# Performance work log

Hardware: AMD Instinct MI355X
Metric: run time of the kernel (lower is better)

## Reference

```python
import jax, jax.numpy as jnp
import numpy as np

K = 3.0  # power parameter k from __init__

def _weight1_sq(d2, r):
    # weight1 on squared distances: (1 - (d/r)^2)^k where d < r, else 0
    r2 = r * r
    flag = d2 < r2
    base = jnp.where(flag, 1.0 - d2 / r2, 0.0)  # >= 0 where flag
    return jnp.where(flag, base ** K, 0.0)

def _weight2(d, r):
    half = r * 0.5
    in1 = d < half
    in2 = (d >= half) & (d < r)
    d_safe = jnp.where(in2, d, half)  # keep base in [0,1] outside the branch
    t = (2.0 * d_safe - r) / r
    w2 = (1.0 - t * t) ** K
    return jnp.where(in1, 1.0, jnp.where(in2, w2, 0.0))

def _normalize(w):
    return w / jnp.sum(w, axis=0, keepdims=True)


def setup_inputs() -> dict:
    key = jax.random.key(0)
    n, p = 4096, 64
    x = jax.random.normal(key, (n, p), dtype=jnp.float32)
    return {
        "x": x,
        "r0": jnp.float32(12.0),
        "r1": jnp.float32(11.0),
        "r2": jnp.float32(12.0),
    }


def reference(x, r0, r1, r2):
    y = x  # y = x.clone(); purely functional here
    sq = jnp.sum(x * x, axis=1)
    # squared pairwise distances (cdist^2), clamped for numerical safety
    d2 = jnp.maximum(sq[:, None] + sq[None, :] - 2.0 * (x @ x.T), 0.0)  # (n, n)
    max_dist = jnp.sqrt(jnp.max(d2))
    # parameter reassignment r := min(r, max_dist)
    r0 = jnp.minimum(r0, max_dist)
    r1 = jnp.minimum(r1, max_dist)
    r2 = jnp.minimum(r2, max_dist)
    # row selection inds: dist[i,i] = 0 <= r0 always, so all rows are kept (identity)
    alpha = _normalize(_weight1_sq(d2, r0))  # (n, n)
    mu = alpha.T @ x  # (n, p)
    mu = jnp.where(jnp.isnan(mu), y, mu)
    U = y - mu  # (n, p), contraction directions
    # projection[i,j] = c_ij * U_j with c_ij = (x_i - y_j) . U_j
    c = x @ U.T - jnp.sum(y * U, axis=1)[None, :]  # (n, n)
    du = c * c * jnp.sum(U * U, axis=1)[None, :]   # ||projection||^2, (n, n)
    du = jnp.maximum(du, 1e-6)
    dv = jnp.sqrt(jnp.maximum(d2 - du, 1e-6))
    du = jnp.sqrt(du)
    beta = _normalize(_weight2(dv, r1) * _weight2(du, r2))  # (n, n)
    e_Z = beta.T @ x  # (n, p)
    return jnp.where(jnp.isnan(e_Z), y, e_Z)
```

## Files before the change

### kernel.cpp

```cpp
#include <hip/hip_runtime.h>
#include <stdint.h>

typedef unsigned short u16;
typedef short bf16x8 __attribute__((ext_vector_type(8)));
typedef unsigned short u16x4 __attribute__((ext_vector_type(4)));
typedef float f32x4 __attribute__((ext_vector_type(4)));

#define NROW 4096
#define LDW 72
#define SLICE 262144
#define NSPLIT 8

__device__ __forceinline__ u16 f2bf(float f) {
  uint32_t u = __float_as_uint(f);
  u = (u + 0x7fffu + ((u >> 16) & 1u)) >> 16;
  return (u16)u;
}

__device__ __forceinline__ u16 f2bf_t(float f) {
  return (u16)(__float_as_uint(f) >> 16);
}

__device__ __forceinline__ f32x4 mfma16(bf16x8 a, bf16x8 b, f32x4 c) {
  return __builtin_amdgcn_mfma_f32_16x16x32_bf16(a, b, c, 0, 0, 0);
}

__device__ __forceinline__ bf16x8 ld8(const u16* p) {
  return *reinterpret_cast<const bf16x8*>(p);
}

__device__ __forceinline__ float fast_sqrt(float x) {
  return __builtin_amdgcn_sqrtf(x);
}

__device__ __forceinline__ float slots_max(const float* __restrict__ maxslots, int lane) {
  float md = maxslots[lane * 16];
#pragma unroll
  for (int o = 1; o < 64; o <<= 1) md = fmaxf(md, __shfl_xor(md, o));
  return md;
}

__global__ __launch_bounds__(256) void prep_kernel(const float* __restrict__ x,
                                                   u16* __restrict__ xb, u16* __restrict__ xT,
                                                   float* __restrict__ sq,
                                                   float* __restrict__ maxslots) {
  __shared__ u16 lt[64 * 68];
  __shared__ float pmax[4];
  const int w = threadIdx.x >> 6, lane = threadIdx.x & 63;
  const int r0 = blockIdx.x * 64;
  const float x0l = x[lane];
  float wmax = 0.f;
#pragma unroll
  for (int rr = 0; rr < 16; ++rr) {
    int rl = w * 16 + rr;
    int row = r0 + rl;
    float v = x[row * 64 + lane];
    u16 b = f2bf(v);
    xb[row * 64 + lane] = b;
    lt[lane * 68 + rl] = b;
    float s = v * v;
    float d = v - x0l;
    float s2 = d * d;
#pragma unroll
    for (int o = 1; o < 64; o <<= 1) {
      s += __shfl_xor(s, o);
      s2 += __shfl_xor(s2, o);
    }
    if (lane == 0) sq[row] = s;
    wmax = fmaxf(wmax, s2);
  }
  if (lane == 0) pmax[w] = wmax;
  __syncthreads();
#pragma unroll
  for (int cc = 0; cc < 16; ++cc) {
    int c = w * 16 + cc;
    xT[c * NROW + r0 + lane] = lt[c * 68 + lane];
  }
  if (threadIdx.x == 0)
    maxslots[blockIdx.x * 16] = fmaxf(fmaxf(pmax[0], pmax[1]), fmaxf(pmax[2], pmax[3]));
}

__global__ __launch_bounds__(256) void pass1_max(const u16* __restrict__ xb,
                                                 const float* __restrict__ sq,
                                                 float* __restrict__ maxslots,
                                                 const float* __restrict__ r0in,
                                                 const float* __restrict__ r1in,
                                                 const float* __restrict__ r2in) {
  __shared__ float red[4];
  int w = threadIdx.x >> 6, lane = threadIdx.x & 63;
  {
    float lb = slots_max(maxslots, lane);
    float rmax = fmaxf(fmaxf(r0in[0], r1in[0]), r2in[0]);
    if (lb >= rmax * rmax) return;
  }
  int l16 = lane & 15, quad = lane >> 4;
  int ti = blockIdx.x;
  int i0 = ti * 64 + w * 16;
  bf16x8 a0 = ld8(xb + (i0 + l16) * 64 + quad * 8);
  bf16x8 a1 = ld8(xb + (i0 + l16) * 64 + 32 + quad * 8);
  float sqi[4];
#pragma unroll
  for (int r = 0; r < 4; ++r) sqi[r] = sq[i0 + quad * 4 + r];
  float m = 0.f;
  const int jbase = blockIdx.y * 256;
#pragma unroll
  for (int jb = 0; jb < 4; ++jb) {
    int j0 = jbase + jb * 64;
#pragma unroll
    for (int jt = 0; jt < 4; ++jt) {
      int jr = j0 + jt * 16 + l16;
      bf16x8 b0 = ld8(xb + jr * 64 + quad * 8);
      bf16x8 b1 = ld8(xb + jr * 64 + 32 + quad * 8);
      f32x4 g = {0.f, 0.f, 0.f, 0.f};
      g = mfma16(a0, b0, g);
      g = mfma16(a1, b1, g);
      float sj = sq[jr];
#pragma unroll
      for (int r = 0; r < 4; ++r) m = fmaxf(m, fmaf(-2.f, g[r], sqi[r] + sj));
    }
  }
  m = fmaxf(m, 0.f);
#pragma unroll
  for (int o = 1; o < 64; o <<= 1) m = fmaxf(m, __shfl_xor(m, o));
  if (lane == 0) red[w] = m;
  __syncthreads();
  if (threadIdx.x == 0) {
    m = fmaxf(fmaxf(red[0], red[1]), fmaxf(red[2], red[3]));
    atomicMax((int*)&maxslots[ti * 16], __float_as_int(m));
  }
}

__global__ __launch_bounds__(256, 2) void pass2_kernel(
    const u16* __restrict__ xb, const u16* __restrict__ xT, const float* __restrict__ sq,
    const float* __restrict__ maxslots, const float* __restrict__ r0in,
    float* __restrict__ mu_part, float* __restrict__ s_part) {
  __shared__ u16 ldsw[2][64 * LDW];
  __shared__ u16 xjt[64 * LDW];
  __shared__ float sred[4][64];
  const int tid = threadIdx.x, w = tid >> 6, lane = tid & 63;
  const int l16 = lane & 15, quad = lane >> 4;
  const int j0 = blockIdx.x * 64;
  const int ibase = blockIdx.y * 512;

#pragma unroll
  for (int k = 0; k < 2; ++k) {
    int ch = tid + k * 256;
    int row = ch >> 3, c8 = ch & 7;
    *reinterpret_cast<bf16x8*>(&xjt[row * LDW + c8 * 8]) = ld8(xb + (j0 + row) * 64 + c8 * 8);
  }

  const float md = slots_max(maxslots, lane);
  const float r0c = fminf(r0in[0], fast_sqrt(md));
  const float invr0sq = 1.f / (r0c * r0c);

  float sqj[4];
#pragma unroll
  for (int jt = 0; jt < 4; ++jt) sqj[jt] = sq[j0 + jt * 16 + l16];

  f32x4 zero4 = {0.f, 0.f, 0.f, 0.f};
  f32x4 acc[4];
#pragma unroll
  for (int pt = 0; pt < 4; ++pt) acc[pt] = zero4;
  float sa[4] = {0.f, 0.f, 0.f, 0.f};

  auto do_weights = [&](bf16x8 A0, bf16x8 A1, float4 QI, u16* wbuf) {
#pragma unroll
    for (int jp = 0; jp < 2; ++jp) {
      const int jt0 = jp * 2, jt1 = jp * 2 + 1;
      f32x4 g0 = zero4, g1 = zero4;
      bf16x8 x00 = ld8(&xjt[(jt0 * 16 + l16) * LDW + quad * 8]);
      bf16x8 x10 = ld8(&xjt[(jt1 * 16 + l16) * LDW + quad * 8]);
      bf16x8 x01 = ld8(&xjt[(jt0 * 16 + l16) * LDW + 32 + quad * 8]);
      bf16x8 x11 = ld8(&xjt[(jt1 * 16 + l16) * LDW + 32 + quad * 8]);
      g0 = mfma16(A0, x00, g0);
      g1 = mfma16(A0, x10, g1);
      g0 = mfma16(A1, x01, g0);
      g1 = mfma16(A1, x11, g1);
      u16x4 pk0, pk1;
#pragma unroll
      for (int r = 0; r < 4; ++r) {
        float d2a = fmaxf(fmaf(-2.f, g0[r], QI[r] + sqj[jt0]), 0.f);
        float ba = fmaxf(fmaf(-d2a, invr0sq, 1.f), 0.f);
        float wa = ba * ba * ba;
        sa[jt0] += wa;
        pk0[r] = f2bf_t(wa);
        float d2b = fmaxf(fmaf(-2.f, g1[r], QI[r] + sqj[jt1]), 0.f);
        float bb = fmaxf(fmaf(-d2b, invr0sq, 1.f), 0.f);
        float wb = bb * bb * bb;
        sa[jt1] += wb;
        pk1[r] = f2bf_t(wb);
      }
      *reinterpret_cast<u16x4*>(&wbuf[(jt0 * 16 + l16) * LDW + w * 16 + quad * 4]) = pk0;
      *reinterpret_cast<u16x4*>(&wbuf[(jt1 * 16 + l16) * LDW + w * 16 + quad * 4]) = pk1;
    }
  };

  const int ir0 = ibase + w * 16;
  bf16x8 p0 = ld8(xb + (ir0 + l16) * 64 + quad * 8);
  bf16x8 p1 = ld8(xb + (ir0 + l16) * 64 + 32 + quad * 8);
  float4 q0 = *reinterpret_cast<const float4*>(&sq[ir0 + quad * 4]);
  __syncthreads();
  do_weights(p0, p1, q0, &ldsw[0][0]);
  bf16x8 a0 = ld8(xb + (ir0 + 64 + l16) * 64 + quad * 8);
  bf16x8 a1 = ld8(xb + (ir0 + 64 + l16) * 64 + 32 + quad * 8);
  float4 qi = *reinterpret_cast<const float4*>(&sq[ir0 + 64 + quad * 4]);
  __syncthreads();

#pragma unroll
  for (int s = 0; s < 8; ++s) {
    u16* rbuf = &ldsw[s & 1][0];
    const int ib = ibase + s * 64;
    bf16x8 aw0 = ld8(&rbuf[(w * 16 + l16) * LDW + quad * 8]);
    bf16x8 aw1 = ld8(&rbuf[(w * 16 + l16) * LDW + 32 + quad * 8]);
    const u16* xp0 = xT + (0 * 16 + l16) * NROW + ib + quad * 8;
    const u16* xp1 = xT + (1 * 16 + l16) * NROW + ib + quad * 8;
    const u16* xp2 = xT + (2 * 16 + l16) * NROW + ib + quad * 8;
    const u16* xp3 = xT + (3 * 16 + l16) * NROW + ib + quad * 8;
    bf16x8 t00 = ld8(xp0), t01 = ld8(xp0 + 32);
    bf16x8 t10 = ld8(xp1), t11 = ld8(xp1 + 32);
    bf16x8 t20 = ld8(xp2), t21 = ld8(xp2 + 32);
    bf16x8 t30 = ld8(xp3), t31 = ld8(xp3 + 32);
    if (s < 7) {
      do_weights(a0, a1, qi, &ldsw[(s + 1) & 1][0]);
      if (s < 6) {
        const int irn = ibase + (s + 2) * 64 + w * 16;
        a0 = ld8(xb + (irn + l16) * 64 + quad * 8);
        a1 = ld8(xb + (irn + l16) * 64 + 32 + quad * 8);
        qi = *reinterpret_cast<const float4*>(&sq[irn + quad * 4]);
      }
    }
    acc[0] = mfma16(aw0, t00, acc[0]);
    acc[0] = mfma16(aw1, t01, acc[0]);
    acc[1] = mfma16(aw0, t10, acc[1]);
    acc[1] = mfma16(aw1, t11, acc[1]);
    acc[2] = mfma16(aw0, t20, acc[2]);
    acc[2] = mfma16(aw1, t21, acc[2]);
    acc[3] = mfma16(aw0, t30, acc[3]);
    acc[3] = mfma16(aw1, t31, acc[3]);
    __syncthreads();
  }
  float* mp = mu_part + (size_t)blockIdx.y * SLICE;
#pragma unroll
  for (int pt = 0; pt < 4; ++pt)
#pragma unroll
    for (int r = 0; r < 4; ++r)
      mp[(j0 + w * 16 + quad * 4 + r) * 64 + pt * 16 + l16] = acc[pt][r];
#pragma unroll
  for (int jt = 0; jt < 4; ++jt) {
    float v = sa[jt];
    v += __shfl_xor(v, 16);
    v += __shfl_xor(v, 32);
    if (lane < 16) sred[w][jt * 16 + lane] = v;
  }
  __syncthreads();
  if (tid < 64)
    s_part[blockIdx.y * NROW + j0 + tid] =
        sred[0][tid] + sred[1][tid] + sred[2][tid] + sred[3][tid];
}

__global__ __launch_bounds__(256) void finish_mu_kernel(
    const float* __restrict__ x, const float* __restrict__ mu_part,
    const float* __restrict__ s_part, u16* __restrict__ ub, float* __restrict__ un2,
    float* __restrict__ tvec) {
  const int tid = threadIdx.x;
  const int row = blockIdx.x * 16 + (tid >> 4);
  const int c4 = tid & 15;
  float4 num = {0.f, 0.f, 0.f, 0.f};
  float den = 0.f;
#pragma unroll
  for (int y = 0; y < NSPLIT; ++y) {
    float4 v = *reinterpret_cast<const float4*>(&mu_part[(size_t)y * SLICE + row * 64 + c4 * 4]);
    num.x += v.x; num.y += v.y; num.z += v.z; num.w += v.w;
    den += s_part[y * NROW + row];
  }
  float4 xv = *reinterpret_cast<const float4*>(&x[row * 64 + c4 * 4]);
  float inv = 1.f / den;
  float m0 = num.x * inv, m1 = num.y * inv, m2 = num.z * inv, m3 = num.w * inv;
  if (m0 != m0) m0 = xv.x;
  if (m1 != m1) m1 = xv.y;
  if (m2 != m2) m2 = xv.z;
  if (m3 != m3) m3 = xv.w;
  float U0 = xv.x - m0, U1 = xv.y - m1, U2 = xv.z - m2, U3 = xv.w - m3;
  u16x4 pb;
  pb[0] = f2bf(U0); pb[1] = f2bf(U1); pb[2] = f2bf(U2); pb[3] = f2bf(U3);
  *reinterpret_cast<u16x4*>(&ub[row * 64 + c4 * 4]) = pb;
  float a = U0 * U0 + U1 * U1 + U2 * U2 + U3 * U3;
  float b = xv.x * U0 + xv.y * U1 + xv.z * U2 + xv.w * U3;
#pragma unroll
  for (int o = 1; o < 16; o <<= 1) {
    a += __shfl_xor(a, o);
    b += __shfl_xor(b, o);
  }
  if (c4 == 0) {
    un2[row] = a;
    tvec[row] = b;
  }
}

__global__ __launch_bounds__(256, 2) void pass3_kernel(
    const u16* __restrict__ xb, const u16* __restrict__ xT, const u16* __restrict__ ub,
    const float* __restrict__ sq, const float* __restrict__ tvec, const float* __restrict__ un2,
    const float* __restrict__ maxslots, const float* __restrict__ r1in,
    const float* __restrict__ r2in, float* __restrict__ ez_part, float* __restrict__ s_part) {
  __shared__ u16 ldsw[2][64 * LDW];
  __shared__ u16 xjt[64 * LDW];
  __shared__ u16 ujt[64 * LDW];
  __shared__ float sred[4][64];
  const int tid = threadIdx.x, w = tid >> 6, lane = tid & 63;
  const int l16 = lane & 15, quad = lane >> 4;
  const int j0 = blockIdx.x * 64;
  const int ibase = blockIdx.y * 512;

#pragma unroll
  for (int k = 0; k < 2; ++k) {
    int ch = tid + k * 256;
    int row = ch >> 3, c8 = ch & 7;
    *reinterpret_cast<bf16x8*>(&xjt[row * LDW + c8 * 8]) = ld8(xb + (j0 + row) * 64 + c8 * 8);
    *reinterpret_cast<bf16x8*>(&ujt[row * LDW + c8 * 8]) = ld8(ub + (j0 + row) * 64 + c8 * 8);
  }

  const float md = slots_max(maxslots, lane);
  const float mdist = fast_sqrt(md);
  const float r1c = fminf(r1in[0], mdist);
  const float r2c = fminf(r2in[0], mdist);
  const float i1x2 = 2.f / r1c;
  const float i2x2 = 2.f / r2c;

  float sqj[4], tj[4], u2j[4];
#pragma unroll
  for (int jt = 0; jt < 4; ++jt) {
    int jr = j0 + jt * 16 + l16;
    sqj[jt] = sq[jr];
    tj[jt] = tvec[jr];
    u2j[jt] = un2[jr];
  }
  f32x4 zero4 = {0.f, 0.f, 0.f, 0.f};
  f32x4 acc[4];
#pragma unroll
  for (int pt = 0; pt < 4; ++pt) acc[pt] = zero4;
  float sb[4] = {0.f, 0.f, 0.f, 0.f};

  auto do_weights = [&](bf16x8 A0, bf16x8 A1, float4 QI, u16* wbuf) {
#pragma unroll
    for (int jt = 0; jt < 4; ++jt) {
      f32x4 gxx = zero4, gxu = zero4;
      bf16x8 xf0 = ld8(&xjt[(jt * 16 + l16) * LDW + quad * 8]);
      bf16x8 uf0 = ld8(&ujt[(jt * 16 + l16) * LDW + quad * 8]);
      bf16x8 xf1 = ld8(&xjt[(jt * 16 + l16) * LDW + 32 + quad * 8]);
      bf16x8 uf1 = ld8(&ujt[(jt * 16 + l16) * LDW + 32 + quad * 8]);
      gxx = mfma16(A0, xf0, gxx);
      gxu = mfma16(A0, uf0, gxu);
      gxx = mfma16(A1, xf1, gxx);
      gxu = mfma16(A1, uf1, gxu);
      const float tjv = tj[jt], u2jv = u2j[jt], sjv = sqj[jt];
      u16x4 pk;
#pragma unroll
      for (int r = 0; r < 4; ++r) {
        float d2 = fmaxf(fmaf(-2.f, gxx[r], QI[r] + sjv), 0.f);
        float c = gxu[r] - tjv;
        float du2 = fmaxf(c * c * u2jv, 1e-6f);
        float dv2 = fmaxf(d2 - du2, 1e-6f);
        float du = fast_sqrt(du2);
        float dv = fast_sqrt(dv2);
        float q1 = fminf(fmaxf(fmaf(dv, i1x2, -1.f), 0.f), 1.f);
        float b1 = fmaf(-q1, q1, 1.f);
        float w1 = b1 * b1 * b1;
        float q2 = fminf(fmaxf(fmaf(du, i2x2, -1.f), 0.f), 1.f);
        float b2 = fmaf(-q2, q2, 1.f);
        float w2 = b2 * b2 * b2;
        float wv = w1 * w2;
        sb[jt] += wv;
        pk[r] = f2bf_t(wv);
      }
      *reinterpret_cast<u16x4*>(&wbuf[(jt * 16 + l16) * LDW + w * 16 + quad * 4]) = pk;
    }
  };

  const int ir0 = ibase + w * 16;
  bf16x8 p0 = ld8(xb + (ir0 + l16) * 64 + quad * 8);
  bf16x8 p1 = ld8(xb + (ir0 + l16) * 64 + 32 + quad * 8);
  float4 q0 = *reinterpret_cast<const float4*>(&sq[ir0 + quad * 4]);
  __syncthreads();
  do_weights(p0, p1, q0, &ldsw[0][0]);
  bf16x8 a0 = ld8(xb + (ir0 + 64 + l16) * 64 + quad * 8);
  bf16x8 a1 = ld8(xb + (ir0 + 64 + l16) * 64 + 32 + quad * 8);
  float4 qi = *reinterpret_cast<const float4*>(&sq[ir0 + 64 + quad * 4]);
  __syncthreads();

#pragma unroll
  for (int s = 0; s < 8; ++s) {
    u16* rbuf = &ldsw[s & 1][0];
    const int ib = ibase + s * 64;
    bf16x8 aw0 = ld8(&rbuf[(w * 16 + l16) * LDW + quad * 8]);
    bf16x8 aw1 = ld8(&rbuf[(w * 16 + l16) * LDW + 32 + quad * 8]);
    const u16* xp0 = xT + (0 * 16 + l16) * NROW + ib + quad * 8;
    const u16* xp1 = xT + (1 * 16 + l16) * NROW + ib + quad * 8;
    const u16* xp2 = xT + (2 * 16 + l16) * NROW + ib + quad * 8;
    const u16* xp3 = xT + (3 * 16 + l16) * NROW + ib + quad * 8;
    bf16x8 t00 = ld8(xp0), t01 = ld8(xp0 + 32);
    bf16x8 t10 = ld8(xp1), t11 = ld8(xp1 + 32);
    bf16x8 t20 = ld8(xp2), t21 = ld8(xp2 + 32);
    bf16x8 t30 = ld8(xp3), t31 = ld8(xp3 + 32);
    if (s < 7) {
      do_weights(a0, a1, qi, &ldsw[(s + 1) & 1][0]);
      if (s < 6) {
        const int irn = ibase + (s + 2) * 64 + w * 16;
        a0 = ld8(xb + (irn + l16) * 64 + quad * 8);
        a1 = ld8(xb + (irn + l16) * 64 + 32 + quad * 8);
        qi = *reinterpret_cast<const float4*>(&sq[irn + quad * 4]);
      }
    }
    acc[0] = mfma16(aw0, t00, acc[0]);
    acc[0] = mfma16(aw1, t01, acc[0]);
    acc[1] = mfma16(aw0, t10, acc[1]);
    acc[1] = mfma16(aw1, t11, acc[1]);
    acc[2] = mfma16(aw0, t20, acc[2]);
    acc[2] = mfma16(aw1, t21, acc[2]);
    acc[3] = mfma16(aw0, t30, acc[3]);
    acc[3] = mfma16(aw1, t31, acc[3]);
    __syncthreads();
  }
  float* ep = ez_part + (size_t)blockIdx.y * SLICE;
#pragma unroll
  for (int pt = 0; pt < 4; ++pt)
#pragma unroll
    for (int r = 0; r < 4; ++r)
      ep[(j0 + w * 16 + quad * 4 + r) * 64 + pt * 16 + l16] = acc[pt][r];
#pragma unroll
  for (int jt = 0; jt < 4; ++jt) {
    float v = sb[jt];
    v += __shfl_xor(v, 16);
    v += __shfl_xor(v, 32);
    if (lane < 16) sred[w][jt * 16 + lane] = v;
  }
  __syncthreads();
  if (tid < 64)
    s_part[blockIdx.y * NROW + j0 + tid] =
        sred[0][tid] + sred[1][tid] + sred[2][tid] + sred[3][tid];
}

__global__ __launch_bounds__(256) void finish_kernel(const float* __restrict__ x,
                                                     const float* __restrict__ ez_part,
                                                     const float* __restrict__ s_part,
                                                     float* __restrict__ out) {
  const int tid = threadIdx.x;
  const int row = blockIdx.x * 16 + (tid >> 4);
  const int c4 = tid & 15;
  float4 num = {0.f, 0.f, 0.f, 0.f};
  float den = 0.f;
#pragma unroll
  for (int y = 0; y < NSPLIT; ++y) {
    float4 v = *reinterpret_cast<const float4*>(&ez_part[(size_t)y * SLICE + row * 64 + c4 * 4]);
    num.x += v.x; num.y += v.y; num.z += v.z; num.w += v.w;
    den += s_part[y * NROW + row];
  }
  float4 xv = *reinterpret_cast<const float4*>(&x[row * 64 + c4 * 4]);
  float inv = 1.f / den;
  float4 o;
  o.x = num.x * inv; o.y = num.y * inv; o.z = num.z * inv; o.w = num.w * inv;
  if (o.x != o.x) o.x = xv.x;
  if (o.y != o.y) o.y = xv.y;
  if (o.z != o.z) o.z = xv.z;
  if (o.w != o.w) o.w = xv.w;
  *reinterpret_cast<float4*>(&out[row * 64 + c4 * 4]) = o;
}

extern "C" void kernel_launch(void* const* d_in, const int* in_sizes, int n_in,
                              void* d_out, int out_size, void* d_ws, size_t ws_size,
                              hipStream_t stream) {
  (void)in_sizes; (void)n_in; (void)out_size;
  const float* x = (const float*)d_in[0];
  const float* r0 = (const float*)d_in[1];
  const float* r1 = (const float*)d_in[2];
  const float* r2 = (const float*)d_in[3];
  float* out = (float*)d_out;
  char* ws = (char*)d_ws;

  u16* xb = (u16*)(ws);
  u16* xT = (u16*)(ws + (512 << 10));
  u16* ub = (u16*)(ws + (1024 << 10));
  float* sq = (float*)(ws + (1536 << 10));
  float* tv = (float*)(ws + (1552 << 10));
  float* u2 = (float*)(ws + (1568 << 10));
  float* maxslots = (float*)(ws + (1584 << 10));
  float* s_part_a = (float*)(ws + (1588 << 10));
  float* s_part_b = (float*)(ws + (1844 << 10));
  float* part = (float*)(ws + (2100 << 10));
  size_t need = ((size_t)2100 << 10) + ((size_t)8 << 20);
  if (ws_size < need) return;

  prep_kernel<<<64, 256, 0, stream>>>(x, xb, xT, sq, maxslots);
  pass1_max<<<dim3(64, 16), 256, 0, stream>>>(xb, sq, maxslots, r0, r1, r2);
  pass2_kernel<<<dim3(64, NSPLIT), 256, 0, stream>>>(xb, xT, sq, maxslots, r0, part, s_part_a);
  finish_mu_kernel<<<256, 256, 0, stream>>>(x, part, s_part_a, ub, u2, tv);
  pass3_kernel<<<dim3(64, NSPLIT), 256, 0, stream>>>(xb, xT, ub, sq, tv, u2, maxslots, r1, r2,
                                                     part, s_part_b);
  finish_kernel<<<256, 256, 0, stream>>>(x, part, s_part_b, out);
}
```

Measured before the change: 127.3 us.

## Fuse all six passes into one cooperative persistent kernel with grid syncs

Replaces the six separate kernel launches (prep, max pass, mu pass, finish_mu, beta pass, finish) with a single cooperative kernel of 512 blocks that separates the phases with grid.sync(). This removes per-launch overhead and the gaps between kernels. The old multi-kernel path is kept as a fallback if the cooperative launch fails. The cost is six grid-wide barriers, idle blocks in the phases that use fewer blocks, and a dependence on all 512 blocks being co-resident at two blocks per CU.

```diff
diff --git a/kernel.cpp b/kernel.cpp
--- a/kernel.cpp
+++ b/kernel.cpp
@@ -1,5 +1,8 @@
 #include <hip/hip_runtime.h>
+#include <hip/hip_cooperative_groups.h>
 #include <stdint.h>
+
+namespace cg = cooperative_groups;
 
 typedef unsigned short u16;
 typedef short bf16x8 __attribute__((ext_vector_type(8)));
@@ -33,12 +36,421 @@
   return __builtin_amdgcn_sqrtf(x);
 }
 
-__device__ __forceinline__ float slots_max(const float* __restrict__ maxslots, int lane) {
+__device__ __forceinline__ float slots_max(const float* maxslots, int lane) {
   float md = maxslots[lane * 16];
 #pragma unroll
   for (int o = 1; o < 64; o <<= 1) md = fmaxf(md, __shfl_xor(md, o));
   return md;
 }
+
+__global__ __launch_bounds__(256, 2) void fused_all(
+    const float* __restrict__ x, const float* __restrict__ r0in,
+    const float* __restrict__ r1in, const float* __restrict__ r2in,
+    float* __restrict__ out, u16* __restrict__ xb, u16* __restrict__ xT,
+    u16* __restrict__ ub, float* __restrict__ sq, float* __restrict__ tvec,
+    float* __restrict__ un2, float* maxslots, float* __restrict__ s_part_a,
+    float* __restrict__ s_part_b, float* part ) {
+  cg::grid_group grid = cg::this_grid();
+  __shared__ u16 smem[4 * 64 * LDW];
+  __shared__ float sred[4][64];
+  u16* ldsw0 = smem;
+  u16* ldsw1 = smem + 64 * LDW;
+  u16* xjt = smem + 2 * 64 * LDW;
+  u16* ujt = smem + 3 * 64 * LDW;
+  const int gid = blockIdx.x;
+  const int tid = threadIdx.x, w = tid >> 6, lane = tid & 63;
+  const int l16 = lane & 15, quad = lane >> 4;
+  const int j0 = (gid & 63) * 64;
+  const int yb = gid >> 6;
+  const int ibase = yb * 512;
+  f32x4 zero4 = {0.f, 0.f, 0.f, 0.f};
+
+  if (gid < 64) {
+    u16* lt = smem;
+    const int r0 = gid * 64;
+    const float x0l = x[lane];
+    float wmax = 0.f;
+#pragma unroll
+    for (int rr = 0; rr < 16; ++rr) {
+      int rl = w * 16 + rr;
+      int row = r0 + rl;
+      float v = x[row * 64 + lane];
+      u16 b = f2bf(v);
+      xb[row * 64 + lane] = b;
+      lt[lane * 68 + rl] = b;
+      float s = v * v;
+      float d = v - x0l;
+      float s2 = d * d;
+#pragma unroll
+      for (int o = 1; o < 64; o <<= 1) {
+        s += __shfl_xor(s, o);
+        s2 += __shfl_xor(s2, o);
+      }
+      if (lane == 0) sq[row] = s;
+      wmax = fmaxf(wmax, s2);
+    }
+    if (lane == 0) sred[0][w] = wmax;
+    __syncthreads();
+#pragma unroll
+    for (int cc = 0; cc < 16; ++cc) {
+      int c = w * 16 + cc;
+      xT[c * NROW + r0 + lane] = lt[c * 68 + lane];
+    }
+    if (tid == 0)
+      maxslots[gid * 16] =
+          fmaxf(fmaxf(sred[0][0], sred[0][1]), fmaxf(sred[0][2], sred[0][3]));
+  }
+  grid.sync();
+
+  {
+    float lb = slots_max(maxslots, lane);
+    float rmax = fmaxf(fmaxf(r0in[0], r1in[0]), r2in[0]);
+    if (lb < rmax * rmax) {
+      for (int uu = 0; uu < 2; ++uu) {
+        int u = gid * 2 + uu;
+        int ti = u & 63, yy = u >> 6;
+        int i0 = ti * 64 + w * 16;
+        bf16x8 a0 = ld8(xb + (i0 + l16) * 64 + quad * 8);
+        bf16x8 a1 = ld8(xb + (i0 + l16) * 64 + 32 + quad * 8);
+        float sqi[4];
+#pragma unroll
+        for (int r = 0; r < 4; ++r) sqi[r] = sq[i0 + quad * 4 + r];
+        float m = 0.f;
+        const int jbase = yy * 256;
+#pragma unroll
+        for (int jb = 0; jb < 4; ++jb) {
+          int jj0 = jbase + jb * 64;
+#pragma unroll
+          for (int jt = 0; jt < 4; ++jt) {
+            int jr = jj0 + jt * 16 + l16;
+            bf16x8 b0 = ld8(xb + jr * 64 + quad * 8);
+            bf16x8 b1 = ld8(xb + jr * 64 + 32 + quad * 8);
+            f32x4 g = zero4;
+            g = mfma16(a0, b0, g);
+            g = mfma16(a1, b1, g);
+            float sj = sq[jr];
+#pragma unroll
+            for (int r = 0; r < 4; ++r) m = fmaxf(m, fmaf(-2.f, g[r], sqi[r] + sj));
+          }
+        }
+        m = fmaxf(m, 0.f);
+#pragma unroll
+        for (int o = 1; o < 64; o <<= 1) m = fmaxf(m, __shfl_xor(m, o));
+        if (lane == 0) sred[0][w] = m;
+        __syncthreads();
+        if (tid == 0) {
+          m = fmaxf(fmaxf(sred[0][0], sred[0][1]), fmaxf(sred[0][2], sred[0][3]));
+          atomicMax((int*)&maxslots[ti * 16], __float_as_int(m));
+        }
+        __syncthreads();
+      }
+    }
+  }
+  grid.sync();
+
+  {
+#pragma unroll
+    for (int k = 0; k < 2; ++k) {
+      int ch = tid + k * 256;
+      int row = ch >> 3, c8 = ch & 7;
+      *reinterpret_cast<bf16x8*>(&xjt[row * LDW + c8 * 8]) =
+          ld8(xb + (j0 + row) * 64 + c8 * 8);
+    }
+    const float md = slots_max(maxslots, lane);
+    const float r0c = fminf(r0in[0], fast_sqrt(md));
+    const float invr0sq = 1.f / (r0c * r0c);
+    float sqj[4];
+#pragma unroll
+    for (int jt = 0; jt < 4; ++jt) sqj[jt] = sq[j0 + jt * 16 + l16];
+    f32x4 acc[4];
+#pragma unroll
+    for (int pt = 0; pt < 4; ++pt) acc[pt] = zero4;
+    float sa[4] = {0.f, 0.f, 0.f, 0.f};
+    u16* bufs[2] = {ldsw0, ldsw1};
+
+    auto do_weights = [&](bf16x8 A0, bf16x8 A1, float4 QI, u16* wbuf) {
+#pragma unroll
+      for (int jp = 0; jp < 2; ++jp) {
+        const int jt0 = jp * 2, jt1 = jp * 2 + 1;
+        f32x4 g0 = zero4, g1 = zero4;
+        bf16x8 x00 = ld8(&xjt[(jt0 * 16 + l16) * LDW + quad * 8]);
+        bf16x8 x10 = ld8(&xjt[(jt1 * 16 + l16) * LDW + quad * 8]);
+        bf16x8 x01 = ld8(&xjt[(jt0 * 16 + l16) * LDW + 32 + quad * 8]);
+        bf16x8 x11 = ld8(&xjt[(jt1 * 16 + l16) * LDW + 32 + quad * 8]);
+        g0 = mfma16(A0, x00, g0);
+        g1 = mfma16(A0, x10, g1);
+        g0 = mfma16(A1, x01, g0);
+        g1 = mfma16(A1, x11, g1);
+        u16x4 pk0, pk1;
+#pragma unroll
+        for (int r = 0; r < 4; ++r) {
+          float d2a = fmaxf(fmaf(-2.f, g0[r], QI[r] + sqj[jt0]), 0.f);
+          float ba = fmaxf(fmaf(-d2a, invr0sq, 1.f), 0.f);
+          float wa = ba * ba * ba;
+          sa[jt0] += wa;
+          pk0[r] = f2bf_t(wa);
+          float d2b = fmaxf(fmaf(-2.f, g1[r], QI[r] + sqj[jt1]), 0.f);
+          float bb = fmaxf(fmaf(-d2b, invr0sq, 1.f), 0.f);
+          float wb = bb * bb * bb;
+          sa[jt1] += wb;
+          pk1[r] = f2bf_t(wb);
+        }
+        *reinterpret_cast<u16x4*>(&wbuf[(jt0 * 16 + l16) * LDW + w * 16 + quad * 4]) = pk0;
+        *reinterpret_cast<u16x4*>(&wbuf[(jt1 * 16 + l16) * LDW + w * 16 + quad * 4]) = pk1;
+      }
+    };
+
+    const int ir0 = ibase + w * 16;
+    bf16x8 p0 = ld8(xb + (ir0 + l16) * 64 + quad * 8);
+    bf16x8 p1 = ld8(xb + (ir0 + l16) * 64 + 32 + quad * 8);
+    float4 q0 = *reinterpret_cast<const float4*>(&sq[ir0 + quad * 4]);
+    __syncthreads();
+    do_weights(p0, p1, q0, bufs[0]);
+    bf16x8 a0 = ld8(xb + (ir0 + 64 + l16) * 64 + quad * 8);
+    bf16x8 a1 = ld8(xb + (ir0 + 64 + l16) * 64 + 32 + quad * 8);
+    float4 qi = *reinterpret_cast<const float4*>(&sq[ir0 + 64 + quad * 4]);
+    __syncthreads();
+
+#pragma unroll
+    for (int s = 0; s < 8; ++s) {
+      u16* rbuf = bufs[s & 1];
+      const int ib = ibase + s * 64;
+      bf16x8 aw0 = ld8(&rbuf[(w * 16 + l16) * LDW + quad * 8]);
+      bf16x8 aw1 = ld8(&rbuf[(w * 16 + l16) * LDW + 32 + quad * 8]);
+      const u16* xp0 = xT + (0 * 16 + l16) * NROW + ib + quad * 8;
+      const u16* xp1 = xT + (1 * 16 + l16) * NROW + ib + quad * 8;
+      const u16* xp2 = xT + (2 * 16 + l16) * NROW + ib + quad * 8;
+      const u16* xp3 = xT + (3 * 16 + l16) * NROW + ib + quad * 8;
+      bf16x8 t00 = ld8(xp0), t01 = ld8(xp0 + 32);
+      bf16x8 t10 = ld8(xp1), t11 = ld8(xp1 + 32);
+      bf16x8 t20 = ld8(xp2), t21 = ld8(xp2 + 32);
+      bf16x8 t30 = ld8(xp3), t31 = ld8(xp3 + 32);
+      if (s < 7) {
+        do_weights(a0, a1, qi, bufs[(s + 1) & 1]);
+        if (s < 6) {
+          const int irn = ibase + (s + 2) * 64 + w * 16;
+          a0 = ld8(xb + (irn + l16) * 64 + quad * 8);
+          a1 = ld8(xb + (irn + l16) * 64 + 32 + quad * 8);
+          qi = *reinterpret_cast<const float4*>(&sq[irn + quad * 4]);
+        }
+      }
+      acc[0] = mfma16(aw0, t00, acc[0]);
+      acc[0] = mfma16(aw1, t01, acc[0]);
+      acc[1] = mfma16(aw0, t10, acc[1]);
+      acc[1] = mfma16(aw1, t11, acc[1]);
+      acc[2] = mfma16(aw0, t20, acc[2]);
+      acc[2] = mfma16(aw1, t21, acc[2]);
+      acc[3] = mfma16(aw0, t30, acc[3]);
+      acc[3] = mfma16(aw1, t31, acc[3]);
+      __syncthreads();
+    }
+    float* mp = part + (size_t)yb * SLICE;
+#pragma unroll
+    for (int pt = 0; pt < 4; ++pt)
+#pragma unroll
+      for (int r = 0; r < 4; ++r)
+        mp[(j0 + w * 16 + quad * 4 + r) * 64 + pt * 16 + l16] = acc[pt][r];
+#pragma unroll
+    for (int jt = 0; jt < 4; ++jt) {
+      float v = sa[jt];
+      v += __shfl_xor(v, 16);
+      v += __shfl_xor(v, 32);
+      if (lane < 16) sred[w][jt * 16 + lane] = v;
+    }
+    __syncthreads();
+    if (tid < 64)
+      s_part_a[yb * NROW + j0 + tid] =
+          sred[0][tid] + sred[1][tid] + sred[2][tid] + sred[3][tid];
+  }
+  grid.sync();
+
+  if (gid < 256) {
+    const int row = gid * 16 + (tid >> 4);
+    const int c4 = tid & 15;
+    float4 num = {0.f, 0.f, 0.f, 0.f};
+    float den = 0.f;
+#pragma unroll
+    for (int y = 0; y < NSPLIT; ++y) {
+      float4 v = *reinterpret_cast<const float4*>(&part[(size_t)y * SLICE + row * 64 + c4 * 4]);
+      num.x += v.x; num.y += v.y; num.z += v.z; num.w += v.w;
+      den += s_part_a[y * NROW + row];
+    }
+    float4 xv = *reinterpret_cast<const float4*>(&x[row * 64 + c4 * 4]);
+    float inv = 1.f / den;
+    float m0 = num.x * inv, m1 = num.y * inv, m2 = num.z * inv, m3 = num.w * inv;
+    if (m0 != m0) m0 = xv.x;
+    if (m1 != m1) m1 = xv.y;
+    if (m2 != m2) m2 = xv.z;
+    if (m3 != m3) m3 = xv.w;
+    float U0 = xv.x - m0, U1 = xv.y - m1, U2 = xv.z - m2, U3 = xv.w - m3;
+    u16x4 pb;
+    pb[0] = f2bf(U0); pb[1] = f2bf(U1); pb[2] = f2bf(U2); pb[3] = f2bf(U3);
+    *reinterpret_cast<u16x4*>(&ub[row * 64 + c4 * 4]) = pb;
+    float a = U0 * U0 + U1 * U1 + U2 * U2 + U3 * U3;
+    float b = xv.x * U0 + xv.y * U1 + xv.z * U2 + xv.w * U3;
+#pragma unroll
+    for (int o = 1; o < 16; o <<= 1) {
+      a += __shfl_xor(a, o);
+      b += __shfl_xor(b, o);
+    }
+    if (c4 == 0) {
+      un2[row] = a;
+      tvec[row] = b;
+    }
+  }
+  grid.sync();
+
+  {
+#pragma unroll
+    for (int k = 0; k < 2; ++k) {
+      int ch = tid + k * 256;
+      int row = ch >> 3, c8 = ch & 7;
+      *reinterpret_cast<bf16x8*>(&ujt[row * LDW + c8 * 8]) =
+          ld8(ub + (j0 + row) * 64 + c8 * 8);
+    }
+    const float md = slots_max(maxslots, lane);
+    const float mdist = fast_sqrt(md);
+    const float r1c = fminf(r1in[0], mdist);
+    const float r2c = fminf(r2in[0], mdist);
+    const float i1x2 = 2.f / r1c;
+    const float i2x2 = 2.f / r2c;
+    float sqj[4], tj[4], u2j[4];
+#pragma unroll
+    for (int jt = 0; jt < 4; ++jt) {
+      int jr = j0 + jt * 16 + l16;
+      sqj[jt] = sq[jr];
+      tj[jt] = tvec[jr];
+      u2j[jt] = un2[jr];
+    }
+    f32x4 acc[4];
+#pragma unroll
+    for (int pt = 0; pt < 4; ++pt) acc[pt] = zero4;
+    float sb[4] = {0.f, 0.f, 0.f, 0.f};
+    u16* bufs[2] = {ldsw0, ldsw1};
+
+    auto do_weights = [&](bf16x8 A0, bf16x8 A1, float4 QI, u16* wbuf) {
+#pragma unroll
+      for (int jt = 0; jt < 4; ++jt) {
+        f32x4 gxx = zero4, gxu = zero4;
+        bf16x8 xf0 = ld8(&xjt[(jt * 16 + l16) * LDW + quad * 8]);
+        bf16x8 uf0 = ld8(&ujt[(jt * 16 + l16) * LDW + quad * 8]);
+        bf16x8 xf1 = ld8(&xjt[(jt * 16 + l16) * LDW + 32 + quad * 8]);
+        bf16x8 uf1 = ld8(&ujt[(jt * 16 + l16) * LDW + 32 + quad * 8]);
+        gxx = mfma16(A0, xf0, gxx);
+        gxu = mfma16(A0, uf0, gxu);
+        gxx = mfma16(A1, xf1, gxx);
+        gxu = mfma16(A1, uf1, gxu);
+        const float tjv = tj[jt], u2jv = u2j[jt], sjv = sqj[jt];
+        u16x4 pk;
+#pragma unroll
+        for (int r = 0; r < 4; ++r) {
+          float d2 = fmaxf(fmaf(-2.f, gxx[r], QI[r] + sjv), 0.f);
+          float c = gxu[r] - tjv;
+          float du2 = fmaxf(c * c * u2jv, 1e-6f);
+          float dv2 = fmaxf(d2 - du2, 1e-6f);
+          float du = fast_sqrt(du2);
+          float dv = fast_sqrt(dv2);
+          float q1 = fminf(fmaxf(fmaf(dv, i1x2, -1.f), 0.f), 1.f);
+          float b1 = fmaf(-q1, q1, 1.f);
+          float w1 = b1 * b1 * b1;
+          float q2 = fminf(fmaxf(fmaf(du, i2x2, -1.f), 0.f), 1.f);
+          float b2 = fmaf(-q2, q2, 1.f);
+          float w2 = b2 * b2 * b2;
+          float wv = w1 * w2;
+          sb[jt] += wv;
+          pk[r] = f2bf_t(wv);
+        }
+        *reinterpret_cast<u16x4*>(&wbuf[(jt * 16 + l16) * LDW + w * 16 + quad * 4]) = pk;
+      }
+    };
+
+    const int ir0 = ibase + w * 16;
+    bf16x8 p0 = ld8(xb + (ir0 + l16) * 64 + quad * 8);
+    bf16x8 p1 = ld8(xb + (ir0 + l16) * 64 + 32 + quad * 8);
+    float4 q0 = *reinterpret_cast<const float4*>(&sq[ir0 + quad * 4]);
+    __syncthreads();
+    do_weights(p0, p1, q0, bufs[0]);
+    bf16x8 a0 = ld8(xb + (ir0 + 64 + l16) * 64 + quad * 8);
+    bf16x8 a1 = ld8(xb + (ir0 + 64 + l16) * 64 + 32 + quad * 8);
+    float4 qi = *reinterpret_cast<const float4*>(&sq[ir0 + 64 + quad * 4]);
+    __syncthreads();
+
+#pragma unroll
+    for (int s = 0; s < 8; ++s) {
+      u16* rbuf = bufs[s & 1];
+      const int ib = ibase + s * 64;
+      bf16x8 aw0 = ld8(&rbuf[(w * 16 + l16) * LDW + quad * 8]);
+      bf16x8 aw1 = ld8(&rbuf[(w * 16 + l16) * LDW + 32 + quad * 8]);
+      const u16* xp0 = xT + (0 * 16 + l16) * NROW + ib + quad * 8;
+      const u16* xp1 = xT + (1 * 16 + l16) * NROW + ib + quad * 8;
+      const u16* xp2 = xT + (2 * 16 + l16) * NROW + ib + quad * 8;
+      const u16* xp3 = xT + (3 * 16 + l16) * NROW + ib + quad * 8;
+      bf16x8 t00 = ld8(xp0), t01 = ld8(xp0 + 32);
+      bf16x8 t10 = ld8(xp1), t11 = ld8(xp1 + 32);
+      bf16x8 t20 = ld8(xp2), t21 = ld8(xp2 + 32);
+      bf16x8 t30 = ld8(xp3), t31 = ld8(xp3 + 32);
+      if (s < 7) {
+        do_weights(a0, a1, qi, bufs[(s + 1) & 1]);
+        if (s < 6) {
+          const int irn = ibase + (s + 2) * 64 + w * 16;
+          a0 = ld8(xb + (irn + l16) * 64 + quad * 8);
+          a1 = ld8(xb + (irn + l16) * 64 + 32 + quad * 8);
+          qi = *reinterpret_cast<const float4*>(&sq[irn + quad * 4]);
+        }
+      }
+      acc[0] = mfma16(aw0, t00, acc[0]);
+      acc[0] = mfma16(aw1, t01, acc[0]);
+      acc[1] = mfma16(aw0, t10, acc[1]);
+      acc[1] = mfma16(aw1, t11, acc[1]);
+      acc[2] = mfma16(aw0, t20, acc[2]);
+      acc[2] = mfma16(aw1, t21, acc[2]);
+      acc[3] = mfma16(aw0, t30, acc[3]);
+      acc[3] = mfma16(aw1, t31, acc[3]);
+      __syncthreads();
+    }
+    float* ep = part + (size_t)yb * SLICE;
+#pragma unroll
+    for (int pt = 0; pt < 4; ++pt)
+#pragma unroll
+      for (int r = 0; r < 4; ++r)
+        ep[(j0 + w * 16 + quad * 4 + r) * 64 + pt * 16 + l16] = acc[pt][r];
+#pragma unroll
+    for (int jt = 0; jt < 4; ++jt) {
+      float v = sb[jt];
+      v += __shfl_xor(v, 16);
+      v += __shfl_xor(v, 32);
+      if (lane < 16) sred[w][jt * 16 + lane] = v;
+    }
+    __syncthreads();
+    if (tid < 64)
+      s_part_b[yb * NROW + j0 + tid] =
+          sred[0][tid] + sred[1][tid] + sred[2][tid] + sred[3][tid];
+  }
+  grid.sync();
+
+  if (gid < 256) {
+    const int row = gid * 16 + (tid >> 4);
+    const int c4 = tid & 15;
+    float4 num = {0.f, 0.f, 0.f, 0.f};
+    float den = 0.f;
+#pragma unroll
+    for (int y = 0; y < NSPLIT; ++y) {
+      float4 v = *reinterpret_cast<const float4*>(&part[(size_t)y * SLICE + row * 64 + c4 * 4]);
+      num.x += v.x; num.y += v.y; num.z += v.z; num.w += v.w;
+      den += s_part_b[y * NROW + row];
+    }
+    float4 xv = *reinterpret_cast<const float4*>(&x[row * 64 + c4 * 4]);
+    float inv = 1.f / den;
+    float4 o;
+    o.x = num.x * inv; o.y = num.y * inv; o.z = num.z * inv; o.w = num.w * inv;
+    if (o.x != o.x) o.x = xv.x;
+    if (o.y != o.y) o.y = xv.y;
+    if (o.z != o.z) o.z = xv.z;
+    if (o.w != o.w) o.w = xv.w;
+    *reinterpret_cast<float4*>(&out[row * 64 + c4 * 4]) = o;
+  }
+}
+
 
 __global__ __launch_bounds__(256) void prep_kernel(const float* __restrict__ x,
                                                    u16* __restrict__ xb, u16* __restrict__ xT,
@@ -141,28 +553,23 @@
   const int l16 = lane & 15, quad = lane >> 4;
   const int j0 = blockIdx.x * 64;
   const int ibase = blockIdx.y * 512;
-
 #pragma unroll
   for (int k = 0; k < 2; ++k) {
     int ch = tid + k * 256;
     int row = ch >> 3, c8 = ch & 7;
     *reinterpret_cast<bf16x8*>(&xjt[row * LDW + c8 * 8]) = ld8(xb + (j0 + row) * 64 + c8 * 8);
   }
-
   const float md = slots_max(maxslots, lane);
   const float r0c = fminf(r0in[0], fast_sqrt(md));
   const float invr0sq = 1.f / (r0c * r0c);
-
   float sqj[4];
 #pragma unroll
   for (int jt = 0; jt < 4; ++jt) sqj[jt] = sq[j0 + jt * 16 + l16];
-
   f32x4 zero4 = {0.f, 0.f, 0.f, 0.f};
   f32x4 acc[4];
 #pragma unroll
   for (int pt = 0; pt < 4; ++pt) acc[pt] = zero4;
   float sa[4] = {0.f, 0.f, 0.f, 0.f};
-
   auto do_weights = [&](bf16x8 A0, bf16x8 A1, float4 QI, u16* wbuf) {
 #pragma unroll
     for (int jp = 0; jp < 2; ++jp) {
@@ -194,7 +601,6 @@
       *reinterpret_cast<u16x4*>(&wbuf[(jt1 * 16 + l16) * LDW + w * 16 + quad * 4]) = pk1;
     }
   };
-
   const int ir0 = ibase + w * 16;
   bf16x8 p0 = ld8(xb + (ir0 + l16) * 64 + quad * 8);
   bf16x8 p1 = ld8(xb + (ir0 + l16) * 64 + 32 + quad * 8);
@@ -205,7 +611,6 @@
   bf16x8 a1 = ld8(xb + (ir0 + 64 + l16) * 64 + 32 + quad * 8);
   float4 qi = *reinterpret_cast<const float4*>(&sq[ir0 + 64 + quad * 4]);
   __syncthreads();
-
 #pragma unroll
   for (int s = 0; s < 8; ++s) {
     u16* rbuf = &ldsw[s & 1][0];
@@ -310,7 +715,6 @@
   const int l16 = lane & 15, quad = lane >> 4;
   const int j0 = blockIdx.x * 64;
   const int ibase = blockIdx.y * 512;
-
 #pragma unroll
   for (int k = 0; k < 2; ++k) {
     int ch = tid + k * 256;
@@ -318,14 +722,12 @@
     *reinterpret_cast<bf16x8*>(&xjt[row * LDW + c8 * 8]) = ld8(xb + (j0 + row) * 64 + c8 * 8);
     *reinterpret_cast<bf16x8*>(&ujt[row * LDW + c8 * 8]) = ld8(ub + (j0 + row) * 64 + c8 * 8);
   }
-
   const float md = slots_max(maxslots, lane);
   const float mdist = fast_sqrt(md);
   const float r1c = fminf(r1in[0], mdist);
   const float r2c = fminf(r2in[0], mdist);
   const float i1x2 = 2.f / r1c;
   const float i2x2 = 2.f / r2c;
-
   float sqj[4], tj[4], u2j[4];
 #pragma unroll
   for (int jt = 0; jt < 4; ++jt) {
@@ -339,7 +741,6 @@
 #pragma unroll
   for (int pt = 0; pt < 4; ++pt) acc[pt] = zero4;
   float sb[4] = {0.f, 0.f, 0.f, 0.f};
-
   auto do_weights = [&](bf16x8 A0, bf16x8 A1, float4 QI, u16* wbuf) {
 #pragma unroll
     for (int jt = 0; jt < 4; ++jt) {
@@ -375,7 +776,6 @@
       *reinterpret_cast<u16x4*>(&wbuf[(jt * 16 + l16) * LDW + w * 16 + quad * 4]) = pk;
     }
   };
-
   const int ir0 = ibase + w * 16;
   bf16x8 p0 = ld8(xb + (ir0 + l16) * 64 + quad * 8);
   bf16x8 p1 = ld8(xb + (ir0 + l16) * 64 + 32 + quad * 8);
@@ -386,7 +786,6 @@
   bf16x8 a1 = ld8(xb + (ir0 + 64 + l16) * 64 + 32 + quad * 8);
   float4 qi = *reinterpret_cast<const float4*>(&sq[ir0 + 64 + quad * 4]);
   __syncthreads();
-
 #pragma unroll
   for (int s = 0; s < 8; ++s) {
     u16* rbuf = &ldsw[s & 1][0];
@@ -489,11 +888,19 @@
   size_t need = ((size_t)2100 << 10) + ((size_t)8 << 20);
   if (ws_size < need) return;
 
-  prep_kernel<<<64, 256, 0, stream>>>(x, xb, xT, sq, maxslots);
-  pass1_max<<<dim3(64, 16), 256, 0, stream>>>(xb, sq, maxslots, r0, r1, r2);
-  pass2_kernel<<<dim3(64, NSPLIT), 256, 0, stream>>>(xb, xT, sq, maxslots, r0, part, s_part_a);
-  finish_mu_kernel<<<256, 256, 0, stream>>>(x, part, s_part_a, ub, u2, tv);
-  pass3_kernel<<<dim3(64, NSPLIT), 256, 0, stream>>>(xb, xT, ub, sq, tv, u2, maxslots, r1, r2,
-                                                     part, s_part_b);
-  finish_kernel<<<256, 256, 0, stream>>>(x, part, s_part_b, out);
-}
+  void* kargs[] = {(void*)&x,  (void*)&r0,  (void*)&r1,       (void*)&r2,
+                   (void*)&out, (void*)&xb,  (void*)&xT,       (void*)&ub,
+                   (void*)&sq,  (void*)&tv,  (void*)&u2,       (void*)&maxslots,
+                   (void*)&s_part_a, (void*)&s_part_b, (void*)&part};
+  hipError_t e = hipLaunchCooperativeKernel((const void*)fused_all, dim3(512), dim3(256),
+                                            kargs, 0, stream);
+  if (e != hipSuccess) {
+    prep_kernel<<<64, 256, 0, stream>>>(x, xb, xT, sq, maxslots);
+    pass1_max<<<dim3(64, 16), 256, 0, stream>>>(xb, sq, maxslots, r0, r1, r2);
+    pass2_kernel<<<dim3(64, NSPLIT), 256, 0, stream>>>(xb, xT, sq, maxslots, r0, part, s_part_a);
+    finish_mu_kernel<<<256, 256, 0, stream>>>(x, part, s_part_a, ub, u2, tv);
+    pass3_kernel<<<dim3(64, NSPLIT), 256, 0, stream>>>(xb, xT, ub, sq, tv, u2, maxslots, r1, r2,
+                                                       part, s_part_b);
+    finish_kernel<<<256, 256, 0, stream>>>(x, part, s_part_b, out);
+  }
+}
```

Measured after the change: 400.8 us. 215% more time.
